# Kernel tuning notes

Hardware: AMD Instinct MI355X
Metric: run time of the kernel (lower is better)

Reference implementation:

```python
import jax, jax.numpy as jnp
import numpy as np

NEG_SLOPE = 0.01  # nn.LeakyReLU default

def leaky_relu(v):
    return jnp.where(v >= 0, v, NEG_SLOPE * v)

def setup_inputs() -> dict:
    key = jax.random.key(0)
    ks = jax.random.split(key, 7)
    B, T, I, H, O = 64, 1024, 512, 1024, 512
    x = jax.random.normal(ks[0], (B, T, I), dtype=jnp.float32)
    # Linear params (stored as [in, out] for x @ W + b)
    W_in = jax.random.normal(ks[1], (I, H), dtype=jnp.float32) * (1.0 / np.sqrt(I))
    b_in = jax.random.normal(ks[2], (H,), dtype=jnp.float32) * 0.01
    W_h = jax.random.normal(ks[3], (2 * H, H), dtype=jnp.float32) * (1.0 / np.sqrt(2 * H))
    b_h = jax.random.normal(ks[4], (H,), dtype=jnp.float32) * 0.01
    W_out = jax.random.normal(ks[5], (H, O), dtype=jnp.float32) * (1.0 / np.sqrt(H))
    b_out = jax.random.normal(ks[6], (O,), dtype=jnp.float32) * 0.01
    return {"x": x, "W_in": W_in, "b_in": b_in, "W_h": W_h, "b_h": b_h,
            "W_out": W_out, "b_out": b_out}

def reference(x, W_in, b_in, W_h, b_h, W_out, b_out):
    B, T, I = x.shape
    H = W_in.shape[1]
    # Precompute input projection for all timesteps in one big GEMM:
    # [B,T,I] @ [I,H] -> [B,T,H], then LeakyReLU.
    h_new_all = leaky_relu(jnp.einsum('bti,ih->bth', x, W_in) + b_in)
    h0 = jnp.zeros((B, H), dtype=x.dtype)

    def step(h, h_new_t):
        combined = jnp.concatenate((h_new_t, h), axis=1)  # [B, 2H]
        h_next = leaky_relu(combined @ W_h + b_h)          # [B, H]
        return h_next, None

    # scan over time axis (sequential dependency on h); dropout_rate=0 => identity
    h_final, _ = jax.lax.scan(step, h0, jnp.swapaxes(h_new_all, 0, 1))
    out = h_final @ W_out + b_out  # [B, O]
    return out
```

## Files before the change

### kernel.cpp

```cpp
#include <hip/hip_runtime.h>
#include <hip/hip_bf16.h>

typedef __attribute__((ext_vector_type(8))) short  s16x8;
typedef __attribute__((ext_vector_type(4))) float  f32x4;
typedef __attribute__((ext_vector_type(4))) unsigned short u16x4;
typedef __attribute__((ext_vector_type(4))) unsigned int   u32x4;

#define B_  64
#define T_  1024
#define I_  512
#define H_  1024
#define O_  512
#define MT_ 65536
#define G2_ 4096

#define RG_   8
#define CS_   16

__device__ __forceinline__ unsigned short f2bf(float f) {
    unsigned u = __builtin_bit_cast(unsigned, f);
    u += 0x7FFFu + ((u >> 16) & 1u);
    return (unsigned short)(u >> 16);
}
__device__ __forceinline__ float bf2f(unsigned short h) {
    return __builtin_bit_cast(float, ((unsigned)h) << 16);
}
__device__ __forceinline__ void store_out(float* p, float v) { *p = v; }
__device__ __forceinline__ void store_out(unsigned short* p, float v) { *p = f2bf(v); }

#define GL2LDS16(gp, lp) __builtin_amdgcn_global_load_lds( \
    (const __attribute__((address_space(1))) void*)(gp),   \
    (__attribute__((address_space(3))) void*)(lp), 16, 0, 0)

__global__ void cvt_x(const float* __restrict__ src, unsigned short* __restrict__ dst, int n) {
    int stride = gridDim.x * blockDim.x * 4;
    for (int i = (blockIdx.x * blockDim.x + threadIdx.x) * 4; i < n; i += stride) {
        const float4 v = *(const float4*)(src + i);
        u16x4 o;
        o.x = f2bf(v.x); o.y = f2bf(v.y); o.z = f2bf(v.z); o.w = f2bf(v.w);
        *(u16x4*)(dst + i) = o;
    }
}

__global__ void cvt_t(const float* __restrict__ src, unsigned short* __restrict__ dst,
                      int SR, int SC, int row_off) {
    __shared__ unsigned short tile[32][33];
    int c0 = blockIdx.x * 32, r0 = blockIdx.y * 32;
    int tx = threadIdx.x, ty = threadIdx.y;
    #pragma unroll
    for (int i = 0; i < 32; i += 8)
        tile[ty + i][tx] = f2bf(src[(size_t)(row_off + r0 + ty + i) * SC + c0 + tx]);
    __syncthreads();
    #pragma unroll
    for (int i = 0; i < 32; i += 8)
        dst[(size_t)(c0 + ty + i) * SR + r0 + tx] = tile[tx][ty + i];
}

__global__ void strip_h(const unsigned* __restrict__ src, unsigned short* __restrict__ dst) {
    int idx = blockIdx.x * blockDim.x + threadIdx.x;
    u32x4 v = *(const u32x4*)(src + idx * 4);
    int rg = idx >> 11, c2 = idx & 2047;
    int q = c2 >> 9, c3 = c2 & 511;
    int j = c3 >> 6, c = c3 & 63;
    int p = c >> 5, a = (c >> 3) & 3, row = c & 7;
    int grow = rg * 8 + row;
    int col = q * 256 + j * 32 + a * 8 + p * 4;
    u16x4 o;
    o.x = (unsigned short)(v.x >> 16); o.y = (unsigned short)(v.y >> 16);
    o.z = (unsigned short)(v.z >> 16); o.w = (unsigned short)(v.w >> 16);
    *(u16x4*)(dst + (size_t)grow * H_ + col) = o;
}

template<typename OutT, bool LRELU>
__global__ __launch_bounds__(256)
void gemm_bf16(const unsigned short* __restrict__ A,
               const unsigned short* __restrict__ BT,
               const float* __restrict__ bias,
               OutT* __restrict__ C, int M, int K, int N)
{
    __shared__ unsigned short As[4096];
    __shared__ unsigned short Bs[4096];
    const int tid = threadIdx.x, lane = tid & 63, wid = tid >> 6;
    const int wr = wid >> 1, wc = wid & 1;
    const int m0 = blockIdx.x * 128, n0 = blockIdx.y * 128;

    f32x4 acc[4][4] = {};

    const int c = wid * 2;
    const int srow = lane >> 2;
    const int scol = (lane & 3) * 8;
    const unsigned short* Ag0 = A  + (size_t)(m0 + c * 16 + srow) * K + scol;
    const unsigned short* Ag1 = A  + (size_t)(m0 + c * 16 + 16 + srow) * K + scol;
    const unsigned short* Bg0 = BT + (size_t)(n0 + c * 16 + srow) * K + scol;
    const unsigned short* Bg1 = BT + (size_t)(n0 + c * 16 + 16 + srow) * K + scol;

    for (int k0 = 0; k0 < K; k0 += 32) {
        __syncthreads();
        GL2LDS16(Ag0 + k0, As + c * 512);
        GL2LDS16(Ag1 + k0, As + (c + 1) * 512);
        GL2LDS16(Bg0 + k0, Bs + c * 512);
        GL2LDS16(Bg1 + k0, Bs + (c + 1) * 512);
        __syncthreads();

        s16x8 af[4], bfr[4];
        #pragma unroll
        for (int i = 0; i < 4; i++)
            af[i] = *(const s16x8*)(As + (wr * 64 + i * 16 + (lane & 15)) * 32 + (lane >> 4) * 8);
        #pragma unroll
        for (int j = 0; j < 4; j++)
            bfr[j] = *(const s16x8*)(Bs + (wc * 64 + j * 16 + (lane & 15)) * 32 + (lane >> 4) * 8);
        #pragma unroll
        for (int i = 0; i < 4; i++)
            #pragma unroll
            for (int j = 0; j < 4; j++)
                acc[i][j] = __builtin_amdgcn_mfma_f32_16x16x32_bf16(af[i], bfr[j], acc[i][j], 0, 0, 0);
    }

    #pragma unroll
    for (int j = 0; j < 4; j++) {
        const int n = n0 + wc * 64 + j * 16 + (lane & 15);
        const float bv = bias[n];
        #pragma unroll
        for (int i = 0; i < 4; i++) {
            #pragma unroll
            for (int r = 0; r < 4; r++) {
                const int m = m0 + wr * 64 + i * 16 + (lane >> 4) * 4 + r;
                if (m < M) {
                    float v = acc[i][j][r] + bv;
                    if (LRELU) v = v >= 0.f ? v : 0.01f * v;
                    store_out(&C[(size_t)m * N + n], v);
                }
            }
        }
    }
}


#define TAGLD2(d, BASE, OFFSTR, SC) asm volatile( \
    "global_load_dwordx4 %0, %1, off offset:" OFFSTR " " SC \
    : "=v"(d) : "v"(BASE))

#define POLLBODY(SC) do { \
    TAGLD2(tv[0],  tA, "0",   SC); TAGLD2(tv[1],  tA, "512",  SC); \
    TAGLD2(tv[2],  tA, "1024",SC); TAGLD2(tv[3],  tA, "1536", SC); \
    TAGLD2(tv[4],  tA, "2048",SC); TAGLD2(tv[5],  tA, "2560", SC); \
    TAGLD2(tv[6],  tA, "3072",SC); TAGLD2(tv[7],  tA, "3584", SC); \
    TAGLD2(tv[8],  tB, "0",   SC); TAGLD2(tv[9],  tB, "512",  SC); \
    TAGLD2(tv[10], tB, "1024",SC); TAGLD2(tv[11], tB, "1536", SC); \
    TAGLD2(tv[12], tB, "2048",SC); TAGLD2(tv[13], tB, "2560", SC); \
    TAGLD2(tv[14], tB, "3072",SC); TAGLD2(tv[15], tB, "3584", SC); \
    } while (0)

#define VALPRE(PV, S) do { \
    unsigned tk = (unsigned)(((PV.x & 0xFFFFu) == 1u) & ((PV.y & 0xFFFFu) == 1u) & \
                             ((PV.z & 0xFFFFu) == 1u) & ((PV.w & 0xFFFFu) == 1u)); \
    while (!__all((int)tk)) { \
        if (!tk) { \
            const unsigned* pp_ = pre32 + ((size_t)(S) * B_ + hrow) * H_ + col0; \
            asm volatile("global_load_dwordx4 %0, %1, off sc0 sc1\n\t" \
                         "s_waitcnt vmcnt(0)" : "=v"(PV) : "v"(pp_) : "memory"); \
            tk = (unsigned)(((PV.x & 0xFFFFu) == 1u) & ((PV.y & 0xFFFFu) == 1u) & \
                            ((PV.z & 0xFFFFu) == 1u) & ((PV.w & 0xFFFFu) == 1u)); \
        } \
        __builtin_amdgcn_s_sleep(2); \
    } } while (0)

#define STEP(S, PVUSE, PVFILL) do { \
    const char* hc32 = (const char*)hbuf32 + (((S) & 1) << 18); \
    char*       hn32 = (char*)hbuf32 + ((((S) + 1) & 1) << 18); \
    const unsigned tagS = (unsigned)(S); \
    const char* tA = hc32 + tbA_off; \
    const char* tB = tA + 4096; \
    float* pb = pbuf + ((S) & 1) * 2176; \
    for (int i_ = 0; i_ < slp; ++i_) __builtin_amdgcn_s_sleep(2); \
    u32x4 tv[16]; \
    unsigned ok = 0u; \
    int rounds_ = 0; \
    for (;;) { \
        if (!ok) { \
            if (!gmode) { POLLBODY("sc0"); } else { POLLBODY("sc0 sc1"); } \
            asm volatile("s_waitcnt vmcnt(0)" ::: "memory"); \
            __builtin_amdgcn_sched_barrier(0); \
            unsigned d_ = 0; \
            _Pragma("unroll") \
            for (int i = 0; i < 16; i++) \
                d_ |= (tv[i].x ^ tagS) | (tv[i].y ^ tagS) | (tv[i].z ^ tagS) | (tv[i].w ^ tagS); \
            ok = ((d_ & 0xFFFFu) == 0u) ? 1u : 0u; \
        } \
        ++rounds_; \
        if (__all((int)ok)) break; \
        if ((rounds_ & 15) == 0) { \
            unsigned fl; \
            asm volatile("global_load_dword %0, %1, off sc0 sc1\n\t" \
                         "s_waitcnt vmcnt(0)" : "=v"(fl) : "v"(dflag) : "memory"); \
            bool anyfl = __any((int)(fl != 0u)); \
            if (!gmode && (anyfl || rounds_ > 96)) { \
                if (!anyfl && lane == 0) { \
                    unsigned one_ = 1u; \
                    asm volatile("global_store_dword %0, %1, off sc0 sc1" \
                                 :: "v"(dflag), "v"(one_) : "memory"); \
                } \
                gmode = 1u; \
                asm volatile("global_store_dwordx4 %0, %1, off sc0 sc1" \
                             :: "v"(lastsp), "v"(lastow) : "memory"); \
            } \
        } \
        __builtin_amdgcn_s_sleep(1); \
    } \
    slp = (rounds_ > 1) ? (slp + 4 > 24 ? 24 : slp + 4) : (slp > 0 ? slp - 1 : 0); \
    { const int sn = ((S) + 1 < T_) ? (S) + 1 : (S); \
      const unsigned* pp_ = pre32 + ((size_t)sn * B_ + hrow) * H_ + col0; \
      asm volatile("global_load_dwordx4 %0, %1, off sc0 sc1" : "=v"(PVFILL) : "v"(pp_)); } \
    f32x4 ac[4] = {}; \
    _Pragma("unroll") \
    for (int cg = 0; cg < 4; ++cg) { \
        const char* pE = wE + cg * 32768; \
        const char* pO = wO + cg * 32768; \
        _Pragma("unroll") \
        for (int j = 0; j < 8; ++j) { \
            u32x4 a2_ = tv[2 * j], b2_ = tv[2 * j + 1]; \
            u32x4 f_; \
            f_.x = (a2_.x >> 16) | (a2_.y & 0xFFFF0000u); \
            f_.y = (a2_.z >> 16) | (a2_.w & 0xFFFF0000u); \
            f_.z = (b2_.x >> 16) | (b2_.y & 0xFFFF0000u); \
            f_.w = (b2_.z >> 16) | (b2_.w & 0xFFFF0000u); \
            s16x8 hfrag = __builtin_bit_cast(s16x8, f_); \
            s16x8 g = *(const s16x8*)(((j & 1) ? pO : pE) + j * 64); \
            ac[cg] = __builtin_amdgcn_mfma_f32_16x16x32_bf16(g, hfrag, ac[cg], 0, 0, 0); \
        } \
    } \
    if (l15 < 8) { \
        float* pw_ = pb + (w * 8 + l15) * 68 + l4 * 4; \
        *(f32x4*)(pw_ +  0) = ac[0]; \
        *(f32x4*)(pw_ + 16) = ac[1]; \
        *(f32x4*)(pw_ + 32) = ac[2]; \
        *(f32x4*)(pw_ + 48) = ac[3]; \
    } \
    asm volatile("s_waitcnt lgkmcnt(0)" ::: "memory"); \
    __builtin_amdgcn_s_barrier(); \
    asm volatile("" ::: "memory"); \
    VALPRE(PVUSE, S); \
    if (l15 < 8) { \
        const float* pr_ = pb + l15 * 68 + w * 16 + l4 * 4; \
        f32x4 s0 = *(const f32x4*)(pr_); \
        f32x4 s1 = *(const f32x4*)(pr_ + 544); \
        f32x4 s2 = *(const f32x4*)(pr_ + 1088); \
        f32x4 s3 = *(const f32x4*)(pr_ + 1632); \
        f32x4 sm = (s0 + s1) + (s2 + s3); \
        u32x4 ow; \
        _Pragma("unroll") \
        for (int r = 0; r < 4; r++) { \
            float v = sm[r] + bf2f((unsigned short)(PVUSE[r] >> 16)); \
            v = v >= 0.f ? v : 0.01f * v; \
            ow[r] = ((unsigned)f2bf(v) << 16) | (tagS + 1u); \
        } \
        char* sp = hn32 + sp_off; \
        if (!gmode) { \
            asm volatile("global_store_dwordx4 %0, %1, off sc0" \
                         :: "v"(sp), "v"(ow) : "memory"); \
        } else { \
            asm volatile("global_store_dwordx4 %0, %1, off sc0 sc1" \
                         :: "v"(sp), "v"(ow) : "memory"); \
        } \
        lastow = ow; lastsp = sp; \
    } \
  } while (0)

__global__ __launch_bounds__(256, 1)
void gemm2_scan(const unsigned short* __restrict__ Abuf,
                const unsigned short* __restrict__ WtopT,
                const float* __restrict__ b_h,
                const unsigned short* __restrict__ WbotT,
                unsigned* __restrict__ pre32,
                unsigned* __restrict__ hbuf32,
                unsigned* __restrict__ dflag)
{
    __shared__ char smem[148480];
    const int bid = (int)blockIdx.x;
    const int tid = threadIdx.x, lane = tid & 63, w = tid >> 6;

    if (bid >= 128) {
        unsigned short* As = (unsigned short*)smem;
        unsigned short* Bs = As + 4096;
        const int g = bid - 128;
        const int tch = g >> 9, b = (g >> 3) & 63, nb = g & 7;
        const int m0 = b * 1024 + tch * 128, n0 = nb * 128;
        const int wr = w >> 1, wc = w & 1;

        f32x4 acc[4][4] = {};
        const int c = w * 2, srow = lane >> 2, scol = (lane & 3) * 8;
        const unsigned short* Ag0 = Abuf  + (size_t)(m0 + c * 16 + srow) * H_ + scol;
        const unsigned short* Ag1 = Abuf  + (size_t)(m0 + c * 16 + 16 + srow) * H_ + scol;
        const unsigned short* Bg0 = WtopT + (size_t)(n0 + c * 16 + srow) * H_ + scol;
        const unsigned short* Bg1 = WtopT + (size_t)(n0 + c * 16 + 16 + srow) * H_ + scol;

        for (int k0 = 0; k0 < H_; k0 += 32) {
            __syncthreads();
            GL2LDS16(Ag0 + k0, As + c * 512);
            GL2LDS16(Ag1 + k0, As + (c + 1) * 512);
            GL2LDS16(Bg0 + k0, Bs + c * 512);
            GL2LDS16(Bg1 + k0, Bs + (c + 1) * 512);
            __syncthreads();

            s16x8 af[4], bfr[4];
            #pragma unroll
            for (int i = 0; i < 4; i++)
                af[i] = *(const s16x8*)(As + (wr * 64 + i * 16 + (lane & 15)) * 32 + (lane >> 4) * 8);
            #pragma unroll
            for (int j = 0; j < 4; j++)
                bfr[j] = *(const s16x8*)(Bs + (wc * 64 + j * 16 + (lane & 15)) * 32 + (lane >> 4) * 8);
            #pragma unroll
            for (int i = 0; i < 4; i++)
                #pragma unroll
                for (int j = 0; j < 4; j++)
                    acc[i][j] = __builtin_amdgcn_mfma_f32_16x16x32_bf16(af[i], bfr[j], acc[i][j], 0, 0, 0);
        }

        #pragma unroll
        for (int j = 0; j < 4; j++) {
            const int n = n0 + wc * 64 + j * 16 + (lane & 15);
            const float bv = b_h[n];
            #pragma unroll
            for (int i = 0; i < 4; i++) {
                #pragma unroll
                for (int r = 0; r < 4; r++) {
                    const int m = m0 + wr * 64 + i * 16 + (lane >> 4) * 4 + r;
                    float v = acc[i][j][r] + bv;
                    size_t row = (size_t)((m & (T_ - 1)) * B_ + (m >> 10));
                    unsigned ow = ((unsigned)f2bf(v) << 16) | 1u;
                    unsigned* p = pre32 + row * H_ + n;
                    asm volatile("global_store_dword %0, %1, off sc0 sc1"
                                 :: "v"(p), "v"(ow) : "memory");
                }
            }
        }
        return;
    }

    unsigned short* Ws = (unsigned short*)smem;
    float* pbuf = (float*)(smem + 131072);
    const int rg = bid & 7;
    const int cs = bid >> 3;
    const int n0 = cs * 64;

    for (int idx = tid; idx < 64 * 128; idx += 256) {
        int r = idx >> 7, kb = (idx & 127) * 16;
        s16x8 v = *(const s16x8*)(WbotT + (size_t)(n0 + r) * H_ + (idx & 127) * 8);
        *(s16x8*)((char*)Ws + r * 2048 + (kb ^ ((r & 7) << 4))) = v;
    }
    __syncthreads();

    const int l15 = lane & 15, l4 = lane >> 4;
    const int hrow = rg * 8 + (l15 & 7);
    const int col0 = n0 + w * 16 + l4 * 4;

    const int tbA_off = rg * 32768 + w * 8192 + (lane >> 4) * 128 + (lane & 7) * 16;
    const int q_ = col0 >> 8, j_ = (col0 >> 5) & 7, a_ = (col0 >> 3) & 3, p_ = (col0 >> 2) & 1;
    const int sp_off = rg * 32768 + q_ * 8192 + j_ * 1024 + p_ * 512 + (a_ * 8 + (l15 & 7)) * 16;

    const int b6 = (l15 >> 2) & 1;
    const char* wsRow = (const char*)Ws + l15 * 2048 + ((l4 * 16) ^ ((l15 & 3) << 4)) + w * 512;
    const char* wE = wsRow + b6 * 64;
    const char* wO = wsRow - b6 * 64;

    int slp = 0;
    unsigned gmode = 0;
    u32x4 lastow = {};
    char* lastsp = (char*)dflag + 1024 + tid * 16;

    u32x4 pvA, pvB;
    {   const unsigned* pp_ = pre32 + (size_t)hrow * H_ + col0;
        asm volatile("global_load_dwordx4 %0, %1, off sc0 sc1" : "=v"(pvA) : "v"(pp_));
        asm volatile("s_waitcnt vmcnt(0)" ::: "memory"); }

    for (int t = 0; t < T_; t += 2) {
        STEP(t,     pvA, pvB);
        STEP(t + 1, pvB, pvA);
    }
}

extern "C" void kernel_launch(void* const* d_in, const int* in_sizes, int n_in,
                              void* d_out, int out_size, void* d_ws, size_t ws_size,
                              hipStream_t stream)
{
    const float* x     = (const float*)d_in[0];
    const float* W_in  = (const float*)d_in[1];
    const float* b_in  = (const float*)d_in[2];
    const float* W_h   = (const float*)d_in[3];
    const float* b_h   = (const float*)d_in[4];
    const float* W_out = (const float*)d_in[5];
    const float* b_out = (const float*)d_in[6];
    float* out = (float*)d_out;

    char* ws = (char*)d_ws;
    size_t off = 0;
    auto alloc = [&](size_t bytes) { void* p = ws + off; off += (bytes + 255) & ~(size_t)255; return p; };

    unsigned short* Xb    = (unsigned short*)alloc((size_t)MT_ * I_ * 2);
    unsigned short* WinT  = (unsigned short*)alloc((size_t)H_ * I_ * 2);
    unsigned short* WtopT = (unsigned short*)alloc((size_t)H_ * H_ * 2);
    unsigned short* WbotT = (unsigned short*)alloc((size_t)H_ * H_ * 2);
    unsigned short* WoutT = (unsigned short*)alloc((size_t)O_ * H_ * 2);
    unsigned short* Abuf  = (unsigned short*)alloc((size_t)MT_ * H_ * 2);
    unsigned*       hbuf32 = (unsigned*)alloc((size_t)2 * B_ * H_ * 4);
    unsigned*       dbuf  = (unsigned*)alloc(8192);
    unsigned short* hfin  = (unsigned short*)alloc((size_t)B_ * H_ * 2);
    unsigned*       pre32 = (unsigned*)alloc((size_t)MT_ * H_ * 4);

    hipMemsetAsync(hbuf32, 0, (size_t)2 * B_ * H_ * 4, stream);
    hipMemsetAsync(dbuf, 0, 8192, stream);
    hipMemsetAsync(pre32, 0, (size_t)MT_ * H_ * 4, stream);

    cvt_x<<<2048, 256, 0, stream>>>(x, Xb, MT_ * I_);
    dim3 tb(32, 8);
    cvt_t<<<dim3(H_ / 32, I_ / 32), tb, 0, stream>>>(W_in,  WinT,  I_, H_, 0);
    cvt_t<<<dim3(H_ / 32, H_ / 32), tb, 0, stream>>>(W_h,   WtopT, H_, H_, 0);
    cvt_t<<<dim3(H_ / 32, H_ / 32), tb, 0, stream>>>(W_h,   WbotT, H_, H_, H_);
    cvt_t<<<dim3(O_ / 32, H_ / 32), tb, 0, stream>>>(W_out, WoutT, H_, O_, 0);

    gemm_bf16<unsigned short, true>
        <<<dim3(MT_ / 128, H_ / 128), 256, 0, stream>>>(Xb, WinT, b_in, Abuf, MT_, I_, H_);

    gemm2_scan<<<128 + G2_, 256, 0, stream>>>(Abuf, WtopT, b_h, WbotT, pre32, hbuf32, dbuf);

    strip_h<<<64, 256, 0, stream>>>(hbuf32, hfin);
    gemm_bf16<float, false>
        <<<dim3(1, O_ / 128), 256, 0, stream>>>(hfin, WoutT, b_out, out, B_, H_, O_);
}
```

Measured before the change: 2.744 ms.

## Replace per-element tagged pre-activation handshake with per-chunk atomic counters

The producer GEMM blocks now write plain bf16 pre-activations instead of 32-bit words carrying a validity tag. Each block bumps an atomic counter per (time chunk, batch group, column group) after its stores drain. Scan blocks wait on that counter once every 128 steps instead of validating tags every step. This halves the pre-activation buffer and its memset, removes per-step validation spinning, and narrows the loads. The cost is coarser waits at chunk boundaries, and correctness now depends on the store/atomic ordering.

```diff
diff --git a/kernel.cpp b/kernel.cpp
--- a/kernel.cpp
+++ b/kernel.cpp
@@ -151,18 +151,14 @@
     TAGLD2(tv[14], tB, "3072",SC); TAGLD2(tv[15], tB, "3584", SC); \
     } while (0)
 
-#define VALPRE(PV, S) do { \
-    unsigned tk = (unsigned)(((PV.x & 0xFFFFu) == 1u) & ((PV.y & 0xFFFFu) == 1u) & \
-                             ((PV.z & 0xFFFFu) == 1u) & ((PV.w & 0xFFFFu) == 1u)); \
-    while (!__all((int)tk)) { \
-        if (!tk) { \
-            const unsigned* pp_ = pre32 + ((size_t)(S) * B_ + hrow) * H_ + col0; \
-            asm volatile("global_load_dwordx4 %0, %1, off sc0 sc1\n\t" \
-                         "s_waitcnt vmcnt(0)" : "=v"(PV) : "v"(pp_) : "memory"); \
-            tk = (unsigned)(((PV.x & 0xFFFFu) == 1u) & ((PV.y & 0xFFFFu) == 1u) & \
-                            ((PV.z & 0xFFFFu) == 1u) & ((PV.w & 0xFFFFu) == 1u)); \
-        } \
-        __builtin_amdgcn_s_sleep(2); \
+#define CNTWAIT(CHK) do { \
+    const unsigned* cp_ = cnt + (CHK) * 64 + rg * 8 + nbq; \
+    unsigned cv_; \
+    for (;;) { \
+        asm volatile("global_load_dword %0, %1, off sc0 sc1\n\t" \
+                     "s_waitcnt vmcnt(0)" : "=v"(cv_) : "v"(cp_) : "memory"); \
+        if (cv_ >= 8u) break; \
+        __builtin_amdgcn_s_sleep(8); \
     } } while (0)
 
 #define STEP(S, PVUSE, PVFILL) do { \
@@ -208,9 +204,10 @@
         __builtin_amdgcn_s_sleep(1); \
     } \
     slp = (rounds_ > 1) ? (slp + 4 > 24 ? 24 : slp + 4) : (slp > 0 ? slp - 1 : 0); \
-    { const int sn = ((S) + 1 < T_) ? (S) + 1 : (S); \
-      const unsigned* pp_ = pre32 + ((size_t)sn * B_ + hrow) * H_ + col0; \
-      asm volatile("global_load_dwordx4 %0, %1, off sc0 sc1" : "=v"(PVFILL) : "v"(pp_)); } \
+    { const int sn_ = ((S) + 1 < T_) ? (S) + 1 : (S); \
+      if (((sn_ & 127) == 0) && ((S) + 1 < T_)) CNTWAIT(sn_ >> 7); \
+      const unsigned short* pp_ = preb + ((size_t)sn_ * B_ + hrow) * H_ + col0; \
+      asm volatile("global_load_dwordx2 %0, %1, off sc0 sc1" : "=v"(PVFILL) : "v"(pp_)); } \
     f32x4 ac[4] = {}; \
     _Pragma("unroll") \
     for (int cg = 0; cg < 4; ++cg) { \
@@ -239,7 +236,6 @@
     asm volatile("s_waitcnt lgkmcnt(0)" ::: "memory"); \
     __builtin_amdgcn_s_barrier(); \
     asm volatile("" ::: "memory"); \
-    VALPRE(PVUSE, S); \
     if (l15 < 8) { \
         const float* pr_ = pb + l15 * 68 + w * 16 + l4 * 4; \
         f32x4 s0 = *(const f32x4*)(pr_); \
@@ -250,7 +246,7 @@
         u32x4 ow; \
         _Pragma("unroll") \
         for (int r = 0; r < 4; r++) { \
-            float v = sm[r] + bf2f((unsigned short)(PVUSE[r] >> 16)); \
+            float v = sm[r] + bf2f((unsigned short)PVUSE[r]); \
             v = v >= 0.f ? v : 0.01f * v; \
             ow[r] = ((unsigned)f2bf(v) << 16) | (tagS + 1u); \
         } \
@@ -271,13 +267,14 @@
                 const unsigned short* __restrict__ WtopT,
                 const float* __restrict__ b_h,
                 const unsigned short* __restrict__ WbotT,
-                unsigned* __restrict__ pre32,
+                unsigned short* __restrict__ preb,
                 unsigned* __restrict__ hbuf32,
                 unsigned* __restrict__ dflag)
 {
     __shared__ char smem[148480];
     const int bid = (int)blockIdx.x;
     const int tid = threadIdx.x, lane = tid & 63, w = tid >> 6;
+    unsigned* cnt = dflag + 1344;
 
     if (bid >= 128) {
         unsigned short* As = (unsigned short*)smem;
@@ -327,13 +324,17 @@
                     const int m = m0 + wr * 64 + i * 16 + (lane >> 4) * 4 + r;
                     float v = acc[i][j][r] + bv;
                     size_t row = (size_t)((m & (T_ - 1)) * B_ + (m >> 10));
-                    unsigned ow = ((unsigned)f2bf(v) << 16) | 1u;
-                    unsigned* p = pre32 + row * H_ + n;
-                    asm volatile("global_store_dword %0, %1, off sc0 sc1"
-                                 :: "v"(p), "v"(ow) : "memory");
+                    unsigned short hv = f2bf(v);
+                    unsigned short* p = preb + row * H_ + n;
+                    asm volatile("global_store_short %0, %1, off sc0 sc1"
+                                 :: "v"(p), "v"(hv) : "memory");
                 }
             }
         }
+        asm volatile("s_waitcnt vmcnt(0)" ::: "memory");
+        if (tid == 0)
+            __hip_atomic_fetch_add(&cnt[tch * 64 + (b >> 3) * 8 + nb], 1u,
+                                   __ATOMIC_RELAXED, __HIP_MEMORY_SCOPE_AGENT);
         return;
     }
 
@@ -342,6 +343,7 @@
     const int rg = bid & 7;
     const int cs = bid >> 3;
     const int n0 = cs * 64;
+    const int nbq = cs >> 1;
 
     for (int idx = tid; idx < 64 * 128; idx += 256) {
         int r = idx >> 7, kb = (idx & 127) * 16;
@@ -368,9 +370,10 @@
     u32x4 lastow = {};
     char* lastsp = (char*)dflag + 1024 + tid * 16;
 
-    u32x4 pvA, pvB;
-    {   const unsigned* pp_ = pre32 + (size_t)hrow * H_ + col0;
-        asm volatile("global_load_dwordx4 %0, %1, off sc0 sc1" : "=v"(pvA) : "v"(pp_));
+    u16x4 pvA, pvB;
+    {   CNTWAIT(0);
+        const unsigned short* pp_ = preb + (size_t)hrow * H_ + col0;
+        asm volatile("global_load_dwordx2 %0, %1, off sc0 sc1" : "=v"(pvA) : "v"(pp_));
         asm volatile("s_waitcnt vmcnt(0)" ::: "memory"); }
 
     for (int t = 0; t < T_; t += 2) {
@@ -405,11 +408,10 @@
     unsigned*       hbuf32 = (unsigned*)alloc((size_t)2 * B_ * H_ * 4);
     unsigned*       dbuf  = (unsigned*)alloc(8192);
     unsigned short* hfin  = (unsigned short*)alloc((size_t)B_ * H_ * 2);
-    unsigned*       pre32 = (unsigned*)alloc((size_t)MT_ * H_ * 4);
+    unsigned short* preb  = (unsigned short*)alloc((size_t)MT_ * H_ * 2);
 
     hipMemsetAsync(hbuf32, 0, (size_t)2 * B_ * H_ * 4, stream);
     hipMemsetAsync(dbuf, 0, 8192, stream);
-    hipMemsetAsync(pre32, 0, (size_t)MT_ * H_ * 4, stream);
 
     cvt_x<<<2048, 256, 0, stream>>>(x, Xb, MT_ * I_);
     dim3 tb(32, 8);
@@ -421,7 +423,7 @@
     gemm_bf16<unsigned short, true>
         <<<dim3(MT_ / 128, H_ / 128), 256, 0, stream>>>(Xb, WinT, b_in, Abuf, MT_, I_, H_);
 
-    gemm2_scan<<<128 + G2_, 256, 0, stream>>>(Abuf, WtopT, b_h, WbotT, pre32, hbuf32, dbuf);
+    gemm2_scan<<<128 + G2_, 256, 0, stream>>>(Abuf, WtopT, b_h, WbotT, preb, hbuf32, dbuf);
 
     strip_h<<<64, 256, 0, stream>>>(hbuf32, hfin);
     gemm_bf16<float, false>
```

Result: faster. 2.639 ms (-3.8%).
